# Kernel optimization log

Hardware: AMD Instinct MI355X
Metric: run time of the kernel (lower is better)

## Reference

```python
import jax, jax.numpy as jnp
import numpy as np

N_NODES = 50000
N_EDGES = 800000
F_IN = 32
H = 128
LN_EPS = 1e-5


def _gcn_layer(h, src, tgt, w_self, b_self, w_neigh, b_neigh):
    # h: [N, D]; src/tgt: [E]
    n = h.shape[0]
    self_feat = h @ w_self + b_self                      # [N, Dout]
    src_feat = h[src]                                    # [E, D] gather
    agg = jax.ops.segment_sum(src_feat, tgt, num_segments=n)          # [N, D]
    cnt = jax.ops.segment_sum(jnp.ones((src.shape[0],), h.dtype), tgt,
                              num_segments=n)[:, None]   # [N, 1]
    agg = agg / jnp.maximum(cnt, 1.0)
    return self_feat + agg @ w_neigh + b_neigh


def _layer_norm(x, gamma, beta):
    mu = jnp.mean(x, axis=-1, keepdims=True)
    var = jnp.mean(jnp.square(x - mu), axis=-1, keepdims=True)
    return (x - mu) * jax.lax.rsqrt(var + LN_EPS) * gamma + beta


def setup_inputs() -> dict:
    key = jax.random.key(0)
    ks = jax.random.split(key, 16)
    s_in = 1.0 / np.sqrt(F_IN)
    s_h = 1.0 / np.sqrt(H)
    inp = {
        "x": jax.random.normal(ks[0], (N_NODES, F_IN), jnp.float32),
        "edge_index": jax.random.randint(ks[1], (2, N_EDGES), 0, N_NODES, jnp.int64)
        if jax.config.jax_enable_x64 else
        jax.random.randint(ks[1], (2, N_EDGES), 0, N_NODES, jnp.int32),
        "w_in": jax.random.uniform(ks[2], (F_IN, H), jnp.float32, -s_in, s_in),
        "b_in": jax.random.uniform(ks[3], (H,), jnp.float32, -s_in, s_in),
        "ws0": jax.random.uniform(ks[4], (H, H), jnp.float32, -s_h, s_h),
        "bs0": jax.random.uniform(ks[5], (H,), jnp.float32, -s_h, s_h),
        "wn0": jax.random.uniform(ks[6], (H, H), jnp.float32, -s_h, s_h),
        "bn0": jax.random.uniform(ks[7], (H,), jnp.float32, -s_h, s_h),
        "g0": jnp.ones((H,), jnp.float32),
        "be0": jnp.zeros((H,), jnp.float32),
        "ws1": jax.random.uniform(ks[8], (H, H), jnp.float32, -s_h, s_h),
        "bs1": jax.random.uniform(ks[9], (H,), jnp.float32, -s_h, s_h),
        "wn1": jax.random.uniform(ks[10], (H, H), jnp.float32, -s_h, s_h),
        "bn1": jax.random.uniform(ks[11], (H,), jnp.float32, -s_h, s_h),
        "g1": jnp.ones((H,), jnp.float32),
        "be1": jnp.zeros((H,), jnp.float32),
    }
    return inp


def reference(x, edge_index, w_in, b_in, ws0, bs0, wn0, bn0, g0, be0,
              ws1, bs1, wn1, bn1, g1, be1):
    src, tgt = edge_index[0], edge_index[1]
    h = jax.nn.relu(x @ w_in + b_in)                     # input_proj + relu
    # layer 0 (intermediate): gcn -> LN -> relu -> dropout(eval=id) -> residual
    residual = h
    h = _gcn_layer(h, src, tgt, ws0, bs0, wn0, bn0)
    h = _layer_norm(h, g0, be0)
    h = jax.nn.relu(h) + residual
    # layer 1 (final): gcn -> LN
    h = _gcn_layer(h, src, tgt, ws1, bs1, wn1, bn1)
    h = _layer_norm(h, g1, be1)
    return h
```

## Files before the change

kernel.cpp:

```cpp
#include <hip/hip_runtime.h>

#define H 128
#define CAP 64
#define FILL_CHUNK 4096
typedef unsigned short ushort_t;
typedef __bf16 bf16x8 __attribute__((ext_vector_type(8)));
typedef float f32x4 __attribute__((ext_vector_type(4)));
typedef float f32x2 __attribute__((ext_vector_type(2)));

__device__ __forceinline__ float bf2f(ushort_t b) {
    return __uint_as_float(((unsigned int)b) << 16);
}
__device__ __forceinline__ ushort_t f2bf(float f) {
    unsigned int u = __float_as_uint(f);
    unsigned int r = (u + 0x7fffu + ((u >> 16) & 1u)) >> 16;
    return (ushort_t)r;
}
__device__ __forceinline__ unsigned char f2fp8(float f) {
    int r = __builtin_amdgcn_cvt_pk_fp8_f32(f, f, 0, false);
    return (unsigned char)(r & 0xff);
}

__device__ __forceinline__
void pack_one(int idx, const float* __restrict__ W0, const float* __restrict__ W1,
              const float* __restrict__ b0, const float* __restrict__ b1,
              ushort_t* __restrict__ Wpack, float* __restrict__ bsum,
              int Ksplit, int K)
{
    int total = K * 16;
    if (idx < total) {
        int l = idx & 63, tt = (idx >> 6) & 7, s = idx >> 9;
        int c = tt * 16 + (l & 15);
        int kb = s * 32 + ((l >> 4) & 3) * 8;
#pragma unroll
        for (int j = 0; j < 8; ++j) {
            int k = kb + j;
            float v = (k < Ksplit) ? W0[(size_t)k * H + c]
                                   : W1[(size_t)(k - Ksplit) * H + c];
            Wpack[(size_t)idx * 8 + j] = f2bf(v);
        }
    }
    if (idx < H) bsum[idx] = b0[idx] + (b1 ? b1[idx] : 0.f);
}

__global__ __launch_bounds__(256)
void k_prep(const float* __restrict__ x, ushort_t* __restrict__ xb, int n4,
            const float* __restrict__ w_in, const float* __restrict__ b_in,
            const float* __restrict__ ws0, const float* __restrict__ bs0,
            const float* __restrict__ wn0, const float* __restrict__ bn0,
            const float* __restrict__ ws1, const float* __restrict__ bs1,
            const float* __restrict__ wn1, const float* __restrict__ bn1,
            ushort_t* __restrict__ Wpin, float* __restrict__ bin,
            ushort_t* __restrict__ Wp0, float* __restrict__ bsm0,
            ushort_t* __restrict__ Wp1, float* __restrict__ bsm1,
            int* __restrict__ fl, int N, int gN)
{
    int b = blockIdx.x, t = threadIdx.x;
    if (b < 2) {
        pack_one(b * 256 + t, w_in, w_in, b_in, nullptr, Wpin, bin, 32, 32);
    } else if (b < 18) {
        pack_one((b - 2) * 256 + t, ws0, wn0, bs0, bn0, Wp0, bsm0, 128, 256);
    } else if (b < 34) {
        pack_one((b - 18) * 256 + t, ws1, wn1, bs1, bn1, Wp1, bsm1, 128, 256);
    } else if (b < 34 + gN) {
        int i = (b - 34) * 256 + t;
        if (i < N) fl[i] = 0;
    } else {
        int i = (b - 34 - gN) * 256 + t;
        if (i < n4) {
            float4 v = ((const float4*)x)[i];
            ushort_t* o = xb + (size_t)i * 4;
            o[0] = f2bf(v.x); o[1] = f2bf(v.y); o[2] = f2bf(v.z); o[3] = f2bf(v.w);
        }
    }
}

template<int K, int DO_LN, int RESREL, int RELU, int OUTBF, int HQ>
__device__ void gemm_body(const ushort_t* __restrict__ A, int lda,
                          const ushort_t* __restrict__ Wpack,
                          const float* __restrict__ bias,
                          const float* __restrict__ g, const float* __restrict__ be,
                          const ushort_t* __restrict__ resid, int ldr,
                          float* __restrict__ Cf, ushort_t* __restrict__ Cb,
                          unsigned char* __restrict__ hq,
                          int ldc, int M, ushort_t* Bs, int bidx, int nb)
{
    constexpr int NS = K / 32;
    const int t = threadIdx.x;
    {
        const uint4* wsrc = (const uint4*)Wpack;
        uint4* wdst = (uint4*)Bs;
        for (int i = t; i < K * 16; i += 256) wdst[i] = wsrc[i];
    }
    __syncthreads();

    const int wave = t >> 6, lane = t & 63;
    const int quad = lane >> 4, l16 = lane & 15;
    const int nt_tiles = (M + 127) / 128;
    const bf16x8* bfr = (const bf16x8*)Bs;

    float bv[8], gv[8], bev[8];
#pragma unroll
    for (int nt = 0; nt < 8; ++nt) {
        int c = nt * 16 + l16;
        bv[nt] = bias[c];
        if (DO_LN) { gv[nt] = g[c]; bev[nt] = be[c]; }
    }

    for (int tile = bidx; tile < nt_tiles; tile += nb) {
        const int m0 = tile * 128 + wave * 32;

        f32x4 acc[2][8];
#pragma unroll
        for (int mt = 0; mt < 2; ++mt)
#pragma unroll
            for (int nt = 0; nt < 8; ++nt) acc[mt][nt] = (f32x4){0.f, 0.f, 0.f, 0.f};

        bf16x8 afrag[NS][2];
#pragma unroll
        for (int s = 0; s < NS; ++s)
#pragma unroll
            for (int mt = 0; mt < 2; ++mt) {
                int row = m0 + mt * 16 + l16;
                if (row >= M) row = M - 1;
                afrag[s][mt] = *(const bf16x8*)(A + (size_t)row * lda + s * 32 + quad * 8);
            }

#pragma unroll
        for (int s = 0; s < NS; ++s)
#pragma unroll
            for (int nt = 0; nt < 8; ++nt) {
                bf16x8 b = bfr[(s * 8 + nt) * 64 + lane];
#pragma unroll
                for (int mt = 0; mt < 2; ++mt)
                    acc[mt][nt] = __builtin_amdgcn_mfma_f32_16x16x32_bf16(
                        afrag[s][mt], b, acc[mt][nt], 0, 0, 0);
            }

#pragma unroll
        for (int mt = 0; mt < 2; ++mt)
#pragma unroll
            for (int r = 0; r < 4; ++r) {
                int row = m0 + mt * 16 + quad * 4 + r;
                float v[8];
#pragma unroll
                for (int nt = 0; nt < 8; ++nt) v[nt] = acc[mt][nt][r] + bv[nt];
                if (DO_LN) {
                    float s1 = 0.f, s2 = 0.f;
#pragma unroll
                    for (int nt = 0; nt < 8; ++nt) { s1 += v[nt]; s2 += v[nt] * v[nt]; }
#pragma unroll
                    for (int mk = 1; mk < 16; mk <<= 1) {
                        s1 += __shfl_xor(s1, mk);
                        s2 += __shfl_xor(s2, mk);
                    }
                    float mu = s1 * (1.f / H);
                    float var = s2 * (1.f / H) - mu * mu;
                    float rs = rsqrtf(var + 1e-5f);
#pragma unroll
                    for (int nt = 0; nt < 8; ++nt)
                        v[nt] = (v[nt] - mu) * rs * gv[nt] + bev[nt];
                }
                if (row < M) {
#pragma unroll
                    for (int nt = 0; nt < 8; ++nt) {
                        int c = nt * 16 + l16;
                        float y = v[nt];
                        if (RELU) y = fmaxf(y, 0.f);
                        if (RESREL)
                            y = fmaxf(y, 0.f) + bf2f(resid[(size_t)row * ldr + c]);
                        if (OUTBF) Cb[(size_t)row * ldc + c] = f2bf(y);
                        else       Cf[(size_t)row * ldc + c] = y;
                        if (HQ) hq[(size_t)row * H + c] = f2fp8(y);
                    }
                }
            }
    }
}

__global__ __launch_bounds__(256)
void k_fill_gin(const int* __restrict__ srcs, const int* __restrict__ tgts,
                int* __restrict__ fl, ushort_t* __restrict__ col, int E, int gF,
                const ushort_t* __restrict__ x_bf,
                const ushort_t* __restrict__ Wpin, const float* __restrict__ bin,
                ushort_t* __restrict__ Acat0, unsigned char* __restrict__ hq0,
                int N, int gM)
{
    __shared__ ushort_t Bs[1 * 8 * 64 * 8];
    if ((int)blockIdx.x < gF) {
        int b = blockIdx.x;
        int range = b & 7;
        int chunk = b >> 3;
        int base = chunk * FILL_CHUNK;
        int lim = base + FILL_CHUNK; if (lim > E) lim = E;
        for (int i = base + (int)threadIdx.x; i < lim; i += 256) {
            int tg = tgts[i];
            if ((tg >> 13) == range) {
                int p = atomicAdd(&fl[tg], 1);
                if (p < CAP) col[tg * CAP + p] = (ushort_t)srcs[i];
            }
        }
    } else {
        gemm_body<32, 0, 0, 1, 1, 1>(x_bf, 32, Wpin, bin,
            nullptr, nullptr, nullptr, 0,
            nullptr, Acat0, hq0, 256, N, Bs, blockIdx.x - gF, gM);
    }
}

template<int DO_LN, int RESREL, int OUTBF, int HQ>
__global__ __launch_bounds__(256)
void k_gemm256(const ushort_t* __restrict__ A,
               const ushort_t* __restrict__ Wpack, const float* __restrict__ bias,
               const float* __restrict__ g, const float* __restrict__ be,
               const ushort_t* __restrict__ resid, int ldr,
               float* __restrict__ Cf, ushort_t* __restrict__ Cb,
               unsigned char* __restrict__ hq, int ldc, int M)
{
    __shared__ ushort_t Bs[8 * 8 * 64 * 8];
    gemm_body<256, DO_LN, RESREL, 0, OUTBF, HQ>(A, 256, Wpack, bias, g, be,
        resid, ldr, Cf, Cb, hq, ldc, M, Bs, blockIdx.x, gridDim.x);
}

__global__ __launch_bounds__(256)
void k_agg(const unsigned char* __restrict__ hq, const int* __restrict__ fl,
           const ushort_t* __restrict__ col, ushort_t* __restrict__ out, int n)
{
    int node = blockIdx.x * 4 + (threadIdx.x >> 6);
    if (node >= n) return;
    int lane = threadIdx.x & 63;
    int grp = lane >> 3, li = lane & 7;
    int cnt = fl[node];
    int m = cnt < CAP ? cnt : CAP;
    int beg = node * CAP;
    float s[16];
#pragma unroll
    for (int j = 0; j < 16; ++j) s[j] = 0.f;

    int e = 0;
    for (; e + 16 <= m; e += 16) {
        int r0 = col[beg + e + grp];
        int r1 = col[beg + e + 8 + grp];
        uint4 v0 = *(const uint4*)(hq + (size_t)r0 * 128 + li * 16);
        uint4 v1 = *(const uint4*)(hq + (size_t)r1 * 128 + li * 16);
        const unsigned int* p0 = (const unsigned int*)&v0;
        const unsigned int* p1 = (const unsigned int*)&v1;
#pragma unroll
        for (int k = 0; k < 4; ++k) {
            f32x2 a0 = __builtin_amdgcn_cvt_pk_f32_fp8(p0[k], false);
            f32x2 a1 = __builtin_amdgcn_cvt_pk_f32_fp8(p0[k], true);
            f32x2 b0 = __builtin_amdgcn_cvt_pk_f32_fp8(p1[k], false);
            f32x2 b1 = __builtin_amdgcn_cvt_pk_f32_fp8(p1[k], true);
            s[4 * k]     += a0.x + b0.x;
            s[4 * k + 1] += a0.y + b0.y;
            s[4 * k + 2] += a1.x + b1.x;
            s[4 * k + 3] += a1.y + b1.y;
        }
    }
    if (e + 8 <= m) {
        int r0 = col[beg + e + grp];
        uint4 v0 = *(const uint4*)(hq + (size_t)r0 * 128 + li * 16);
        const unsigned int* p0 = (const unsigned int*)&v0;
#pragma unroll
        for (int k = 0; k < 4; ++k) {
            f32x2 a0 = __builtin_amdgcn_cvt_pk_f32_fp8(p0[k], false);
            f32x2 a1 = __builtin_amdgcn_cvt_pk_f32_fp8(p0[k], true);
            s[4 * k]     += a0.x;
            s[4 * k + 1] += a0.y;
            s[4 * k + 2] += a1.x;
            s[4 * k + 3] += a1.y;
        }
        e += 8;
    }
    int rem = m - e;
    if (grp < rem) {
        int r0 = col[beg + e + grp];
        uint4 v0 = *(const uint4*)(hq + (size_t)r0 * 128 + li * 16);
        const unsigned int* p0 = (const unsigned int*)&v0;
#pragma unroll
        for (int k = 0; k < 4; ++k) {
            f32x2 a0 = __builtin_amdgcn_cvt_pk_f32_fp8(p0[k], false);
            f32x2 a1 = __builtin_amdgcn_cvt_pk_f32_fp8(p0[k], true);
            s[4 * k]     += a0.x;
            s[4 * k + 1] += a0.y;
            s[4 * k + 2] += a1.x;
            s[4 * k + 3] += a1.y;
        }
    }
#pragma unroll
    for (int j = 0; j < 16; ++j) {
        s[j] += __shfl_xor(s[j], 8);
        s[j] += __shfl_xor(s[j], 16);
        s[j] += __shfl_xor(s[j], 32);
    }
    if (grp == 0) {
        float inv = 1.f / fmaxf((float)cnt, 1.f);
        uint4 o0, o1;
        o0.x = ((unsigned)f2bf(s[1] * inv) << 16)  | f2bf(s[0] * inv);
        o0.y = ((unsigned)f2bf(s[3] * inv) << 16)  | f2bf(s[2] * inv);
        o0.z = ((unsigned)f2bf(s[5] * inv) << 16)  | f2bf(s[4] * inv);
        o0.w = ((unsigned)f2bf(s[7] * inv) << 16)  | f2bf(s[6] * inv);
        o1.x = ((unsigned)f2bf(s[9] * inv) << 16)  | f2bf(s[8] * inv);
        o1.y = ((unsigned)f2bf(s[11] * inv) << 16) | f2bf(s[10] * inv);
        o1.z = ((unsigned)f2bf(s[13] * inv) << 16) | f2bf(s[12] * inv);
        o1.w = ((unsigned)f2bf(s[15] * inv) << 16) | f2bf(s[14] * inv);
        uint4* dst = (uint4*)(out + (size_t)node * 256 + li * 16);
        dst[0] = o0;
        dst[1] = o1;
    }
}

extern "C" void kernel_launch(void* const* d_in, const int* in_sizes, int n_in,
                              void* d_out, int out_size, void* d_ws, size_t ws_size,
                              hipStream_t stream)
{
    const float* x    = (const float*)d_in[0];
    const int*   ei   = (const int*)d_in[1];
    const float* w_in = (const float*)d_in[2];
    const float* b_in = (const float*)d_in[3];
    const float* ws0  = (const float*)d_in[4];
    const float* bs0  = (const float*)d_in[5];
    const float* wn0  = (const float*)d_in[6];
    const float* bn0  = (const float*)d_in[7];
    const float* g0   = (const float*)d_in[8];
    const float* be0  = (const float*)d_in[9];
    const float* ws1  = (const float*)d_in[10];
    const float* bs1  = (const float*)d_in[11];
    const float* wn1  = (const float*)d_in[12];
    const float* bn1  = (const float*)d_in[13];
    const float* g1   = (const float*)d_in[14];
    const float* be1  = (const float*)d_in[15];

    const int N = in_sizes[0] / 32;
    const int E = in_sizes[1] / 2;
    const int* srcs = ei;
    const int* tgts = ei + E;

    char* w = (char*)d_ws;
    ushort_t* Acat0 = (ushort_t*)w;  w += (size_t)N * 256 * 2;
    ushort_t* Acat1 = (ushort_t*)w;  w += (size_t)N * 256 * 2;
    unsigned char* hq0 = (unsigned char*)w;  w += (size_t)N * H;
    unsigned char* hq1 = (unsigned char*)w;  w += (size_t)N * H;
    ushort_t* x_bf  = (ushort_t*)w;  w += (size_t)N * 32 * 2;
    ushort_t* Wpin  = (ushort_t*)w;  w += 32 * H * 2;
    ushort_t* Wp0   = (ushort_t*)w;  w += 256 * H * 2;
    ushort_t* Wp1   = (ushort_t*)w;  w += 256 * H * 2;
    float* bin  = (float*)w;         w += H * 4;
    float* bsm0 = (float*)w;         w += H * 4;
    float* bsm1 = (float*)w;         w += H * 4;
    int* fl     = (int*)w;           w += (size_t)N * 4;
    ushort_t* col = (ushort_t*)w;    w += (size_t)N * CAP * 2;

    int n4 = N * 32 / 4;
    int gN = (N + 255) / 256;
    int gC = (n4 + 255) / 256;
    int gM = (N + 127) / 128;
    int gF = 8 * ((E + FILL_CHUNK - 1) / FILL_CHUNK);

    k_prep<<<34 + gN + gC, 256, 0, stream>>>(
        x, x_bf, n4, w_in, b_in, ws0, bs0, wn0, bn0, ws1, bs1, wn1, bn1,
        Wpin, bin, Wp0, bsm0, Wp1, bsm1, fl, N, gN);

    k_fill_gin<<<gF + gM, 256, 0, stream>>>(
        srcs, tgts, fl, col, E, gF,
        x_bf, Wpin, bin, Acat0, hq0, N, gM);

    k_agg<<<(N + 3) / 4, 256, 0, stream>>>(hq0, fl, col, Acat0 + 128, N);
    k_gemm256<1, 1, 1, 1><<<gM, 256, 0, stream>>>(
        Acat0, Wp0, bsm0, g0, be0, Acat0, 256,
        nullptr, Acat1, hq1, 256, N);

    k_agg<<<(N + 3) / 4, 256, 0, stream>>>(hq1, fl, col, Acat1 + 128, N);
    k_gemm256<1, 0, 0, 0><<<gM, 256, 0, stream>>>(
        Acat1, Wp1, bsm1, g1, be1, nullptr, 0,
        (float*)d_out, nullptr, nullptr, H, N);
}
```

Measured before the change: 237.4 us.

## Use XCD-local work-stealing for edge fill and split GEMM weight staging

The edge-bucketing fill no longer assigns a fixed 8-way range per chunk. It launches 1024 persistent blocks that read their XCD id from a hardware register and claim chunks from a per-XCD atomic ticket counter, so each XCD's atomics on fl/col stay within its own node range. The GEMM loads A fragments first and stages weights in two halves through half-sized LDS, with one tile per block, meant to raise occupancy and overlap the weight load. GEMM blocks now come first in the fused launch. This relies on the XCD register, and correctness assumes no more than 8 XCDs, each handling node range tg>>13.

```diff
diff --git a/kernel.cpp b/kernel.cpp
--- a/kernel.cpp
+++ b/kernel.cpp
@@ -53,10 +53,11 @@
             ushort_t* __restrict__ Wpin, float* __restrict__ bin,
             ushort_t* __restrict__ Wp0, float* __restrict__ bsm0,
             ushort_t* __restrict__ Wp1, float* __restrict__ bsm1,
-            int* __restrict__ fl, int N, int gN)
+            int* __restrict__ fl, int* __restrict__ tick, int N, int gN)
 {
     int b = blockIdx.x, t = threadIdx.x;
     if (b < 2) {
+        if (b == 0 && t < 16) tick[t] = 0;
         pack_one(b * 256 + t, w_in, w_in, b_in, nullptr, Wpin, bin, 32, 32);
     } else if (b < 18) {
         pack_one((b - 2) * 256 + t, ws0, wn0, bs0, bn0, Wp0, bsm0, 128, 256);
@@ -83,21 +84,53 @@
                           const ushort_t* __restrict__ resid, int ldr,
                           float* __restrict__ Cf, ushort_t* __restrict__ Cb,
                           unsigned char* __restrict__ hq,
-                          int ldc, int M, ushort_t* Bs, int bidx, int nb)
+                          int ldc, int M, ushort_t* Bs, int tile)
 {
     constexpr int NS = K / 32;
+    constexpr int HALF = (NS >= 4) ? NS / 2 : NS;
     const int t = threadIdx.x;
-    {
-        const uint4* wsrc = (const uint4*)Wpack;
-        uint4* wdst = (uint4*)Bs;
-        for (int i = t; i < K * 16; i += 256) wdst[i] = wsrc[i];
-    }
-    __syncthreads();
-
     const int wave = t >> 6, lane = t & 63;
     const int quad = lane >> 4, l16 = lane & 15;
-    const int nt_tiles = (M + 127) / 128;
+    const int m0 = tile * 128 + wave * 32;
+
+    bf16x8 afrag[NS][2];
+#pragma unroll
+    for (int s = 0; s < NS; ++s)
+#pragma unroll
+        for (int mt = 0; mt < 2; ++mt) {
+            int row = m0 + mt * 16 + l16;
+            if (row >= M) row = M - 1;
+            afrag[s][mt] = *(const bf16x8*)(A + (size_t)row * lda + s * 32 + quad * 8);
+        }
+
+    f32x4 acc[2][8];
+#pragma unroll
+    for (int mt = 0; mt < 2; ++mt)
+#pragma unroll
+        for (int nt = 0; nt < 8; ++nt) acc[mt][nt] = (f32x4){0.f, 0.f, 0.f, 0.f};
+
     const bf16x8* bfr = (const bf16x8*)Bs;
+#pragma unroll
+    for (int h = 0; h < NS; h += HALF) {
+        __syncthreads();
+        {
+            const uint4* wsrc = (const uint4*)Wpack + h * 512;
+            uint4* wdst = (uint4*)Bs;
+#pragma unroll
+            for (int i = t; i < HALF * 512; i += 256) wdst[i] = wsrc[i];
+        }
+        __syncthreads();
+#pragma unroll
+        for (int s = 0; s < HALF; ++s)
+#pragma unroll
+            for (int nt = 0; nt < 8; ++nt) {
+                bf16x8 b = bfr[(s * 8 + nt) * 64 + lane];
+#pragma unroll
+                for (int mt = 0; mt < 2; ++mt)
+                    acc[mt][nt] = __builtin_amdgcn_mfma_f32_16x16x32_bf16(
+                        afrag[h + s][mt], b, acc[mt][nt], 0, 0, 0);
+            }
+    }
 
     float bv[8], gv[8], bev[8];
 #pragma unroll
@@ -107,103 +140,81 @@
         if (DO_LN) { gv[nt] = g[c]; bev[nt] = be[c]; }
     }
 
-    for (int tile = bidx; tile < nt_tiles; tile += nb) {
-        const int m0 = tile * 128 + wave * 32;
-
-        f32x4 acc[2][8];
-#pragma unroll
-        for (int mt = 0; mt < 2; ++mt)
-#pragma unroll
-            for (int nt = 0; nt < 8; ++nt) acc[mt][nt] = (f32x4){0.f, 0.f, 0.f, 0.f};
-
-        bf16x8 afrag[NS][2];
-#pragma unroll
-        for (int s = 0; s < NS; ++s)
-#pragma unroll
-            for (int mt = 0; mt < 2; ++mt) {
-                int row = m0 + mt * 16 + l16;
-                if (row >= M) row = M - 1;
-                afrag[s][mt] = *(const bf16x8*)(A + (size_t)row * lda + s * 32 + quad * 8);
+#pragma unroll
+    for (int mt = 0; mt < 2; ++mt)
+#pragma unroll
+        for (int r = 0; r < 4; ++r) {
+            int row = m0 + mt * 16 + quad * 4 + r;
+            float v[8];
+#pragma unroll
+            for (int nt = 0; nt < 8; ++nt) v[nt] = acc[mt][nt][r] + bv[nt];
+            if (DO_LN) {
+                float s1 = 0.f, s2 = 0.f;
+#pragma unroll
+                for (int nt = 0; nt < 8; ++nt) { s1 += v[nt]; s2 += v[nt] * v[nt]; }
+#pragma unroll
+                for (int mk = 1; mk < 16; mk <<= 1) {
+                    s1 += __shfl_xor(s1, mk);
+                    s2 += __shfl_xor(s2, mk);
+                }
+                float mu = s1 * (1.f / H);
+                float var = s2 * (1.f / H) - mu * mu;
+                float rs = rsqrtf(var + 1e-5f);
+#pragma unroll
+                for (int nt = 0; nt < 8; ++nt)
+                    v[nt] = (v[nt] - mu) * rs * gv[nt] + bev[nt];
             }
-
-#pragma unroll
-        for (int s = 0; s < NS; ++s)
-#pragma unroll
-            for (int nt = 0; nt < 8; ++nt) {
-                bf16x8 b = bfr[(s * 8 + nt) * 64 + lane];
-#pragma unroll
-                for (int mt = 0; mt < 2; ++mt)
-                    acc[mt][nt] = __builtin_amdgcn_mfma_f32_16x16x32_bf16(
-                        afrag[s][mt], b, acc[mt][nt], 0, 0, 0);
-            }
-
-#pragma unroll
-        for (int mt = 0; mt < 2; ++mt)
-#pragma unroll
-            for (int r = 0; r < 4; ++r) {
-                int row = m0 + mt * 16 + quad * 4 + r;
-                float v[8];
-#pragma unroll
-                for (int nt = 0; nt < 8; ++nt) v[nt] = acc[mt][nt][r] + bv[nt];
-                if (DO_LN) {
-                    float s1 = 0.f, s2 = 0.f;
-#pragma unroll
-                    for (int nt = 0; nt < 8; ++nt) { s1 += v[nt]; s2 += v[nt] * v[nt]; }
-#pragma unroll
-                    for (int mk = 1; mk < 16; mk <<= 1) {
-                        s1 += __shfl_xor(s1, mk);
-                        s2 += __shfl_xor(s2, mk);
-                    }
-                    float mu = s1 * (1.f / H);
-                    float var = s2 * (1.f / H) - mu * mu;
-                    float rs = rsqrtf(var + 1e-5f);
-#pragma unroll
-                    for (int nt = 0; nt < 8; ++nt)
-                        v[nt] = (v[nt] - mu) * rs * gv[nt] + bev[nt];
-                }
-                if (row < M) {
-#pragma unroll
-                    for (int nt = 0; nt < 8; ++nt) {
-                        int c = nt * 16 + l16;
-                        float y = v[nt];
-                        if (RELU) y = fmaxf(y, 0.f);
-                        if (RESREL)
-                            y = fmaxf(y, 0.f) + bf2f(resid[(size_t)row * ldr + c]);
-                        if (OUTBF) Cb[(size_t)row * ldc + c] = f2bf(y);
-                        else       Cf[(size_t)row * ldc + c] = y;
-                        if (HQ) hq[(size_t)row * H + c] = f2fp8(y);
-                    }
+            if (row < M) {
+#pragma unroll
+                for (int nt = 0; nt < 8; ++nt) {
+                    int c = nt * 16 + l16;
+                    float y = v[nt];
+                    if (RELU) y = fmaxf(y, 0.f);
+                    if (RESREL)
+                        y = fmaxf(y, 0.f) + bf2f(resid[(size_t)row * ldr + c]);
+                    if (OUTBF) Cb[(size_t)row * ldc + c] = f2bf(y);
+                    else       Cf[(size_t)row * ldc + c] = y;
+                    if (HQ) hq[(size_t)row * H + c] = f2fp8(y);
                 }
             }
-    }
+        }
 }
 
 __global__ __launch_bounds__(256)
 void k_fill_gin(const int* __restrict__ srcs, const int* __restrict__ tgts,
-                int* __restrict__ fl, ushort_t* __restrict__ col, int E, int gF,
+                int* __restrict__ fl, ushort_t* __restrict__ col,
+                int* __restrict__ tick, int E,
                 const ushort_t* __restrict__ x_bf,
                 const ushort_t* __restrict__ Wpin, const float* __restrict__ bin,
                 ushort_t* __restrict__ Acat0, unsigned char* __restrict__ hq0,
                 int N, int gM)
 {
     __shared__ ushort_t Bs[1 * 8 * 64 * 8];
-    if ((int)blockIdx.x < gF) {
-        int b = blockIdx.x;
-        int range = b & 7;
-        int chunk = b >> 3;
-        int base = chunk * FILL_CHUNK;
-        int lim = base + FILL_CHUNK; if (lim > E) lim = E;
-        for (int i = base + (int)threadIdx.x; i < lim; i += 256) {
-            int tg = tgts[i];
-            if ((tg >> 13) == range) {
-                int p = atomicAdd(&fl[tg], 1);
-                if (p < CAP) col[tg * CAP + p] = (ushort_t)srcs[i];
-            }
-        }
-    } else {
+    __shared__ int schunk;
+    if ((int)blockIdx.x < gM) {
         gemm_body<32, 0, 0, 1, 1, 1>(x_bf, 32, Wpin, bin,
             nullptr, nullptr, nullptr, 0,
-            nullptr, Acat0, hq0, 256, N, Bs, blockIdx.x - gF, gM);
+            nullptr, Acat0, hq0, 256, N, Bs, blockIdx.x);
+    } else {
+        int xcd = __builtin_amdgcn_s_getreg(63508) & 7;
+        int nch = (E + FILL_CHUNK - 1) / FILL_CHUNK;
+        int t = threadIdx.x;
+        for (;;) {
+            if (t == 0) schunk = atomicAdd(&tick[xcd], 1);
+            __syncthreads();
+            int chunk = schunk;
+            __syncthreads();
+            if (chunk >= nch) break;
+            int base = chunk * FILL_CHUNK;
+            int lim = base + FILL_CHUNK; if (lim > E) lim = E;
+            for (int i = base + t; i < lim; i += 256) {
+                int tg = tgts[i];
+                if ((tg >> 13) == xcd) {
+                    int p = atomicAdd(&fl[tg], 1);
+                    if (p < CAP) col[tg * CAP + p] = (ushort_t)srcs[i];
+                }
+            }
+        }
     }
 }
 
@@ -216,9 +227,9 @@
                float* __restrict__ Cf, ushort_t* __restrict__ Cb,
                unsigned char* __restrict__ hq, int ldc, int M)
 {
-    __shared__ ushort_t Bs[8 * 8 * 64 * 8];
+    __shared__ ushort_t Bs[4 * 8 * 64 * 8];
     gemm_body<256, DO_LN, RESREL, 0, OUTBF, HQ>(A, 256, Wpack, bias, g, be,
-        resid, ldr, Cf, Cb, hq, ldc, M, Bs, blockIdx.x, gridDim.x);
+        resid, ldr, Cf, Cb, hq, ldc, M, Bs, blockIdx.x);
 }
 
 __global__ __launch_bounds__(256)
@@ -348,20 +359,21 @@
     float* bsm0 = (float*)w;         w += H * 4;
     float* bsm1 = (float*)w;         w += H * 4;
     int* fl     = (int*)w;           w += (size_t)N * 4;
+    int* tick   = (int*)w;           w += 16 * 4;
     ushort_t* col = (ushort_t*)w;    w += (size_t)N * CAP * 2;
 
     int n4 = N * 32 / 4;
     int gN = (N + 255) / 256;
     int gC = (n4 + 255) / 256;
     int gM = (N + 127) / 128;
-    int gF = 8 * ((E + FILL_CHUNK - 1) / FILL_CHUNK);
+    int gF = 1024;
 
     k_prep<<<34 + gN + gC, 256, 0, stream>>>(
         x, x_bf, n4, w_in, b_in, ws0, bs0, wn0, bn0, ws1, bs1, wn1, bn1,
-        Wpin, bin, Wp0, bsm0, Wp1, bsm1, fl, N, gN);
-
-    k_fill_gin<<<gF + gM, 256, 0, stream>>>(
-        srcs, tgts, fl, col, E, gF,
+        Wpin, bin, Wp0, bsm0, Wp1, bsm1, fl, tick, N, gN);
+
+    k_fill_gin<<<gM + gF, 256, 0, stream>>>(
+        srcs, tgts, fl, col, tick, E,
         x_bf, Wpin, bin, Acat0, hq0, N, gM);
 
     k_agg<<<(N + 3) / 4, 256, 0, stream>>>(hq0, fl, col, Acat0 + 128, N);
```

Result: no change. 236.5 us (-0.4%).
